# Kernel optimization log

Measured on AMD Instinct MI355X. Metric: run time of the kernel, lower is better.

## Reference

```python
import jax, jax.numpy as jnp
import numpy as np

B, IC, OC, K, L = 64, 2, 32, 5, 65536
FS = 50000000.0
J_MAX = 16  # upper bound on resampled kernel length (alpha >= ~0.4 here)
# PERTURB_ORDER = ['CFO','SCALE','GAIN','SHIFT','CHIRP'] -> columns 0..4


def setup_inputs() -> dict:
    key = jax.random.key(0)
    k1, k2, k3, k4 = jax.random.split(key, 4)
    x = jax.random.normal(k1, (B, IC, 1, L), dtype=jnp.float32)
    z = jax.random.randint(k2, (B, 5), 0, 2).astype(jnp.int32)  # perturbation on/off gates
    u = jax.random.uniform(k3, (B, 5), dtype=jnp.float32)
    s = jnp.stack([
        -800.0 + 1600.0 * u[:, 0],   # CFO  (Hz)
        0.8 + 0.5 * u[:, 1],         # SCALE alpha in [0.8, 1.3]
        0.7 + 0.6 * u[:, 2],         # GAIN rho in [0.7, 1.3]
        u[:, 3],                     # SHIFT (unused on kernels)
        -2000.0 + 4000.0 * u[:, 4],  # CHIRP slope
    ], axis=1)
    # kaiming_uniform_(a=0.2, 'relu'... torch uses leaky_relu gain formula with a)
    fan_in = IC * 1 * K
    gain = float(np.sqrt(2.0 / (1.0 + 0.2 ** 2)))
    bound = gain * float(np.sqrt(3.0 / fan_in))
    w0 = jax.random.uniform(k4, (OC, IC, 1, K), minval=-bound, maxval=bound, dtype=jnp.float32)
    return {"x": x, "z": z, "s": s, "w0": w0}


def _resample_matrix(new_W):
    """[K,K] matrix = upsample(new_W->K) @ downsample(K->new_W), linear, align_corners=False."""
    nWf = new_W.astype(jnp.float32)
    # stage 1: K -> new_W  (rows j >= new_W are zero / padded)
    j = jnp.arange(J_MAX, dtype=jnp.float32)
    valid = (j < nWf).astype(jnp.float32)
    src1 = jnp.maximum((j + 0.5) * K / nWf - 0.5, 0.0)
    i0 = jnp.floor(src1).astype(jnp.int32)
    i1 = jnp.minimum(i0 + 1, K - 1)
    lam1 = src1 - i0.astype(jnp.float32)
    eyeK = jnp.eye(K, dtype=jnp.float32)
    W1 = valid[:, None] * ((1.0 - lam1)[:, None] * eyeK[i0] + lam1[:, None] * eyeK[i1])  # [J_MAX,K]
    # stage 2: new_W -> K
    i = jnp.arange(K, dtype=jnp.float32)
    src2 = jnp.maximum((i + 0.5) * nWf / K - 0.5, 0.0)
    j0 = jnp.floor(src2).astype(jnp.int32)
    j1 = jnp.minimum(j0 + 1, new_W - 1)
    lam2 = src2 - j0.astype(jnp.float32)
    eyeJ = jnp.eye(J_MAX, dtype=jnp.float32)
    W2 = (1.0 - lam2)[:, None] * eyeJ[j0] + lam2[:, None] * eyeJ[j1]  # [K,J_MAX]
    return W2 @ W1  # [K,K]


def _rot_iq(w, phi):
    """w: [B,OC,IC,K], phi: [B,K] -> rotate I/Q channels by per-tap phase."""
    I, Q = w[:, :, 0, :], w[:, :, 1, :]
    c = jnp.cos(phi)[:, None, :]
    sn = jnp.sin(phi)[:, None, :]
    return jnp.stack([I * c - Q * sn, I * sn + Q * c], axis=2)


def _forward(x, z, s, w0):
    Bx = x.shape[0]
    Lx = x.shape[-1]
    def param(col, neutral):
        m = z[:, col] > 0
        return jnp.where(m, jnp.nan_to_num(s[:, col]), jnp.float32(neutral))
    alpha = param(1, 1.0)   # coef_scale=1: 1 + 1*(alpha-1) = alpha
    f0 = param(0, 0.0)
    a = param(4, 0.0)
    rho = param(2, 1.0)
    theta = jnp.zeros_like(rho)
    w = jnp.broadcast_to(w0[None, :, :, 0, :], (Bx, OC, IC, K))  # [B,OC,IC,K]
    # SCALE: per-sample down/up linear resample as a [K,K] operator
    new_W = jnp.clip(jnp.round(K / jnp.maximum(alpha, 0.001)), 1, J_MAX).astype(jnp.int32)
    M = jax.vmap(_resample_matrix)(new_W)  # [B,K,K]
    w = jnp.einsum('bxy,boiy->boix', M, w)
    # CFO then CHIRP phase mixing
    n = jnp.arange(K, dtype=jnp.float32)
    w = _rot_iq(w, 2.0 * jnp.pi * f0[:, None] * n / FS)
    w = _rot_iq(w, jnp.pi * a[:, None] * (n / FS) ** 2)
    # GAIN: theta=0 rotation + rho scaling
    cg, sg = jnp.cos(theta)[:, None, None], jnp.sin(theta)[:, None, None]
    I, Q = w[:, :, 0, :], w[:, :, 1, :]
    w = jnp.stack([cg * I - sg * Q, sg * I + cg * Q], axis=2)
    w = rho[:, None, None, None] * w
    # grouped conv: groups = B
    xG = x.reshape(1, Bx * IC, 1, Lx)
    wG = w.reshape(Bx * OC, IC, 1, K)
    yG = jax.lax.conv_general_dilated(
        xG, wG, window_strides=(1, 1), padding=((0, 0), (K // 2, K // 2)),
        dimension_numbers=('NCHW', 'OIHW', 'NCHW'), feature_group_count=Bx)
    return yG.reshape(Bx, OC, 1, Lx)


def reference(x, z, s, w0):
    return _forward(x, z, s, w0)
```

## Files before the change

kernel.cpp:

```cpp
#include <hip/hip_runtime.h>
#include <math.h>
#include <float.h>

constexpr int Bn  = 64;
constexpr int ICn = 2;
constexpr int OCn = 32;
constexpr int Kn  = 5;
constexpr int Ln  = 65536;
constexpr float FSc = 50000000.0f;
constexpr int JMAXn = 16;

constexpr int TPB   = 256;
constexpr int CHUNK = 16384;
constexpr int NCH   = Ln / CHUNK;
constexpr int OCG   = 4;
constexpr int NG    = OCn / OCG;
constexpr int ITERS = CHUNK / (TPB * 4);

typedef float f32x4 __attribute__((ext_vector_type(4)));

__global__ __launch_bounds__(64) void wgen_kernel(const int* __restrict__ z,
                                                  const float* __restrict__ s,
                                                  const float* __restrict__ w0,
                                                  float* __restrict__ w) {
    const int b  = blockIdx.x;
    const int oc = threadIdx.x;
    if (oc >= OCn) return;

    float pv[5];
#pragma unroll
    for (int c = 0; c < 5; ++c) {
        float v = s[b * 5 + c];
        if (isnan(v)) v = 0.0f;
        else if (isinf(v)) v = (v > 0.0f) ? FLT_MAX : -FLT_MAX;
        pv[c] = v;
    }
    const float neutral[5] = {0.0f, 1.0f, 1.0f, 0.0f, 0.0f};
#pragma unroll
    for (int c = 0; c < 5; ++c) {
        if (!(z[b * 5 + c] > 0)) pv[c] = neutral[c];
    }
    const float f0    = pv[0];
    const float alpha = pv[1];
    const float rho   = pv[2];
    const float a     = pv[4];

    float nw = rintf(5.0f / fmaxf(alpha, 0.001f));
    int new_W = (int)nw;
    if (new_W < 1) new_W = 1;
    if (new_W > JMAXn) new_W = JMAXn;
    const float nWf = (float)new_W;

    float M[Kn][Kn];
#pragma unroll
    for (int xi = 0; xi < Kn; ++xi)
#pragma unroll
        for (int y = 0; y < Kn; ++y) M[xi][y] = 0.0f;

#pragma unroll
    for (int xi = 0; xi < Kn; ++xi) {
        const float src2 = fmaxf((xi + 0.5f) * nWf / 5.0f - 0.5f, 0.0f);
        const int   j0   = (int)floorf(src2);
        const int   j1   = min(j0 + 1, new_W - 1);
        const float lam2 = src2 - (float)j0;
        const int   jj[2] = {j0, j1};
        const float cf[2] = {1.0f - lam2, lam2};
#pragma unroll
        for (int t = 0; t < 2; ++t) {
            const int   j  = jj[t];
            const float cc = cf[t];
            const float src1 = fmaxf((j + 0.5f) * 5.0f / nWf - 0.5f, 0.0f);
            const int   i0   = (int)floorf(src1);
            const int   i1   = min(i0 + 1, Kn - 1);
            const float lam1 = src1 - (float)i0;
#pragma unroll
            for (int y = 0; y < Kn; ++y) {
                const float e = ((y == i0) ? (1.0f - lam1) : 0.0f) +
                                ((y == i1) ? lam1 : 0.0f);
                M[xi][y] += cc * e;
            }
        }
    }

    const float* w0b = w0 + oc * (ICn * Kn);
    float wI[Kn], wQ[Kn];
#pragma unroll
    for (int xi = 0; xi < Kn; ++xi) {
        float aI = 0.0f, aQ = 0.0f;
#pragma unroll
        for (int y = 0; y < Kn; ++y) {
            aI += M[xi][y] * w0b[y];
            aQ += M[xi][y] * w0b[Kn + y];
        }
        wI[xi] = aI;
        wQ[xi] = aQ;
    }

    const float c2pi = (float)(2.0 * M_PI);
    const float cpi  = (float)M_PI;
#pragma unroll
    for (int n = 0; n < Kn; ++n) {
        const float nf  = (float)n;
        const float ph1 = ((c2pi * f0) * nf) / FSc;
        const float c1 = cosf(ph1), s1 = sinf(ph1);
        float I = wI[n], Q = wQ[n];
        float I2 = I * c1 - Q * s1;
        float Q2 = I * s1 + Q * c1;
        const float t   = nf / FSc;
        const float ph2 = (cpi * a) * (t * t);
        const float c2 = cosf(ph2), s2 = sinf(ph2);
        float I3 = I2 * c2 - Q2 * s2;
        float Q3 = I2 * s2 + Q2 * c2;
        wI[n] = rho * I3;
        wQ[n] = rho * Q3;
    }

    float* wb = w + (b * OCn + oc) * (ICn * Kn);
#pragma unroll
    for (int k = 0; k < Kn; ++k) {
        wb[k]      = wI[k];
        wb[Kn + k] = wQ[k];
    }
}

__device__ __forceinline__ void fetch_win(const float* __restrict__ x0,
                                          const float* __restrict__ x1,
                                          int l0,
                                          float (&xa)[12], float (&xc)[12]) {
    if (l0 >= 4 && l0 + 8 <= Ln) {
#pragma unroll
        for (int q = 0; q < 3; ++q) {
            const float4 va = *reinterpret_cast<const float4*>(x0 + l0 - 4 + 4 * q);
            const float4 vb = *reinterpret_cast<const float4*>(x1 + l0 - 4 + 4 * q);
            xa[4 * q + 0] = va.x; xa[4 * q + 1] = va.y;
            xa[4 * q + 2] = va.z; xa[4 * q + 3] = va.w;
            xc[4 * q + 0] = vb.x; xc[4 * q + 1] = vb.y;
            xc[4 * q + 2] = vb.z; xc[4 * q + 3] = vb.w;
        }
    } else {
#pragma unroll
        for (int m = 0; m < 12; ++m) {
            const int gl = l0 - 4 + m;
            const bool ok = (gl >= 0 && gl < Ln);
            xa[m] = ok ? x0[gl] : 0.0f;
            xc[m] = ok ? x1[gl] : 0.0f;
        }
    }
}

__device__ __forceinline__ void compute_store(const float (&wv)[OCG][ICn * Kn],
                                              const float (&xa)[12],
                                              const float (&xc)[12],
                                              float* __restrict__ yg, int off) {
#pragma unroll
    for (int j = 0; j < OCG; ++j) {
        float a0 = 0.0f, a1 = 0.0f, a2 = 0.0f, a3 = 0.0f;
#pragma unroll
        for (int k = 0; k < Kn; ++k) {
            const float wA = wv[j][k];
            const float wB = wv[j][Kn + k];
            a0 = fmaf(wA, xa[k + 2], a0); a0 = fmaf(wB, xc[k + 2], a0);
            a1 = fmaf(wA, xa[k + 3], a1); a1 = fmaf(wB, xc[k + 3], a1);
            a2 = fmaf(wA, xa[k + 4], a2); a2 = fmaf(wB, xc[k + 4], a2);
            a3 = fmaf(wA, xa[k + 5], a3); a3 = fmaf(wB, xc[k + 5], a3);
        }
        f32x4 v = {a0, a1, a2, a3};
        __builtin_nontemporal_store(
            v, reinterpret_cast<f32x4*>(yg + (size_t)j * Ln + off));
    }
}

__global__ __launch_bounds__(TPB) void conv_kernel(const float* __restrict__ x,
                                                   const float* __restrict__ w,
                                                   float* __restrict__ y) {
    const int blk   = blockIdx.x;
    const int chunk = blk & (NCH - 1);
    const int g     = (blk >> 2) & (NG - 1);
    const int b     = blk >> 5;
    const int oc0   = g * OCG;

    const float* wbase = w + (size_t)(b * OCn + oc0) * (ICn * Kn);
    float wv[OCG][ICn * Kn];
#pragma unroll
    for (int j = 0; j < OCG; ++j)
#pragma unroll
        for (int i = 0; i < ICn * Kn; ++i) wv[j][i] = wbase[j * (ICn * Kn) + i];

    const float* x0 = x + (size_t)b * (ICn * Ln);
    const float* x1 = x0 + Ln;
    float* yg = y + ((size_t)(b * OCn + oc0)) * Ln + chunk * CHUNK;

    const int l0base  = chunk * CHUNK + (int)threadIdx.x * 4;
    const int offbase = (int)threadIdx.x * 4;

    float xaA[12], xcA[12], xaB[12], xcB[12];

    fetch_win(x0, x1, l0base, xaA, xcA);

#pragma unroll 2
    for (int itp = 0; itp < ITERS; itp += 2) {
        fetch_win(x0, x1, l0base + (itp + 1) * (TPB * 4), xaB, xcB);
        compute_store(wv, xaA, xcA, yg, offbase + itp * (TPB * 4));

        if (itp + 2 < ITERS)
            fetch_win(x0, x1, l0base + (itp + 2) * (TPB * 4), xaA, xcA);
        compute_store(wv, xaB, xcB, yg, offbase + (itp + 1) * (TPB * 4));
    }
}

extern "C" void kernel_launch(void* const* d_in, const int* in_sizes, int n_in,
                              void* d_out, int out_size, void* d_ws, size_t ws_size,
                              hipStream_t stream) {
    const float* x  = (const float*)d_in[0];
    const int*   z  = (const int*)d_in[1];
    const float* s  = (const float*)d_in[2];
    const float* w0 = (const float*)d_in[3];
    float* y = (float*)d_out;
    float* w = (float*)d_ws;

    hipLaunchKernelGGL(wgen_kernel, dim3(Bn), dim3(64), 0, stream, z, s, w0, w);
    hipLaunchKernelGGL(conv_kernel, dim3(Bn * NG * NCH), dim3(TPB), 0, stream, x, w, y);
}
```

Before: 111.0 us.

## Remap conv blocks to iterate over batches instead of length chunks

Each conv block now owns a fixed 1024-sample position range and OC group, and loops over batch samples with a stride of 4 batches, instead of looping over a contiguous length chunk of one batch. Weights are reloaded per iteration because they change with the batch. The grid changes from 2048 blocks to 2048 blocks with the same count (4*8*64). The aim is a different memory access pattern and concurrency of x reuse across OC groups; it adds per-iteration weight loads and large strides between successive accesses.

```diff
diff --git a/kernel.cpp b/kernel.cpp
--- a/kernel.cpp
+++ b/kernel.cpp
@@ -10,12 +10,12 @@
 constexpr float FSc = 50000000.0f;
 constexpr int JMAXn = 16;
 
-constexpr int TPB   = 256;
-constexpr int CHUNK = 16384;
-constexpr int NCH   = Ln / CHUNK;
-constexpr int OCG   = 4;
-constexpr int NG    = OCn / OCG;
-constexpr int ITERS = CHUNK / (TPB * 4);
+constexpr int TPB  = 256;
+constexpr int OCG  = 4;
+constexpr int NG   = OCn / OCG;
+constexpr int BG   = 4;
+constexpr int NIT  = Bn / BG;
+constexpr int NLT  = Ln / (TPB * 4);
 
 typedef float f32x4 __attribute__((ext_vector_type(4)));
 
@@ -148,10 +148,16 @@
     }
 }
 
-__device__ __forceinline__ void compute_store(const float (&wv)[OCG][ICn * Kn],
+__device__ __forceinline__ void compute_store(const float* __restrict__ wbase,
                                               const float (&xa)[12],
                                               const float (&xc)[12],
-                                              float* __restrict__ yg, int off) {
+                                              float* __restrict__ yg, int l0) {
+    float wv[OCG][ICn * Kn];
+#pragma unroll
+    for (int j = 0; j < OCG; ++j)
+#pragma unroll
+        for (int i = 0; i < ICn * Kn; ++i) wv[j][i] = wbase[j * (ICn * Kn) + i];
+
 #pragma unroll
     for (int j = 0; j < OCG; ++j) {
         float a0 = 0.0f, a1 = 0.0f, a2 = 0.0f, a3 = 0.0f;
@@ -166,7 +172,7 @@
         }
         f32x4 v = {a0, a1, a2, a3};
         __builtin_nontemporal_store(
-            v, reinterpret_cast<f32x4*>(yg + (size_t)j * Ln + off));
+            v, reinterpret_cast<f32x4*>(yg + (size_t)j * Ln + l0));
     }
 }
 
@@ -174,37 +180,35 @@
                                                    const float* __restrict__ w,
                                                    float* __restrict__ y) {
     const int blk   = blockIdx.x;
-    const int chunk = blk & (NCH - 1);
-    const int g     = (blk >> 2) & (NG - 1);
-    const int b     = blk >> 5;
+    const int b_off = blk >> 9;
+    const int rblk  = blk & 511;
+    const int g     = rblk >> 6;
+    const int pblk  = rblk & 63;
     const int oc0   = g * OCG;
-
-    const float* wbase = w + (size_t)(b * OCn + oc0) * (ICn * Kn);
-    float wv[OCG][ICn * Kn];
-#pragma unroll
-    for (int j = 0; j < OCG; ++j)
-#pragma unroll
-        for (int i = 0; i < ICn * Kn; ++i) wv[j][i] = wbase[j * (ICn * Kn) + i];
-
-    const float* x0 = x + (size_t)b * (ICn * Ln);
-    const float* x1 = x0 + Ln;
-    float* yg = y + ((size_t)(b * OCn + oc0)) * Ln + chunk * CHUNK;
-
-    const int l0base  = chunk * CHUNK + (int)threadIdx.x * 4;
-    const int offbase = (int)threadIdx.x * 4;
+    const int l0    = (pblk * TPB + (int)threadIdx.x) * 4;
+
+    const size_t xstep = (size_t)BG * ICn * Ln;
+    const size_t wstep = (size_t)BG * OCn * ICn * Kn;
+    const size_t ystep = (size_t)BG * OCn * Ln;
+
+    const float* xp = x + (size_t)b_off * (ICn * Ln);
+    const float* wp = w + (size_t)(b_off * OCn + oc0) * (ICn * Kn);
+    float*       yp = y + (size_t)(b_off * OCn + oc0) * Ln;
 
     float xaA[12], xcA[12], xaB[12], xcB[12];
 
-    fetch_win(x0, x1, l0base, xaA, xcA);
+    fetch_win(xp, xp + Ln, l0, xaA, xcA);
 
 #pragma unroll 2
-    for (int itp = 0; itp < ITERS; itp += 2) {
-        fetch_win(x0, x1, l0base + (itp + 1) * (TPB * 4), xaB, xcB);
-        compute_store(wv, xaA, xcA, yg, offbase + itp * (TPB * 4));
-
-        if (itp + 2 < ITERS)
-            fetch_win(x0, x1, l0base + (itp + 2) * (TPB * 4), xaA, xcA);
-        compute_store(wv, xaB, xcB, yg, offbase + (itp + 1) * (TPB * 4));
+    for (int itp = 0; itp < NIT; itp += 2) {
+        fetch_win(xp + xstep, xp + xstep + Ln, l0, xaB, xcB);
+        compute_store(wp, xaA, xcA, yp, l0);
+        xp += xstep; wp += wstep; yp += ystep;
+
+        if (itp + 2 < NIT)
+            fetch_win(xp + xstep, xp + xstep + Ln, l0, xaA, xcA);
+        compute_store(wp, xaB, xcB, yp, l0);
+        xp += xstep; wp += wstep; yp += ystep;
     }
 }
 
@@ -219,5 +223,6 @@
     float* w = (float*)d_ws;
 
     hipLaunchKernelGGL(wgen_kernel, dim3(Bn), dim3(64), 0, stream, z, s, w0, w);
-    hipLaunchKernelGGL(conv_kernel, dim3(Bn * NG * NCH), dim3(TPB), 0, stream, x, w, y);
-}
+    hipLaunchKernelGGL(conv_kernel, dim3(BG * NG * NLT), dim3(TPB), 0, stream,
+                       x, w, y);
+}
```

New measurement: 108.8 us. -2.0%, faster.
